# Kernel optimization log

Measured on AMD Instinct MI355X. Metric: run time of the kernel, lower is better.

Reference implementation:

```python
import jax, jax.numpy as jnp
import numpy as np

C = 320        # in_channels == inner_dim (n_heads*d_head = 8*40)
HEADS = 8
DH = 40
CTX = 768
FF_INNER = 1280  # 4*C
G = 32         # GroupNorm groups


def _ln(x, w, b, eps=1e-5):
    m = x.mean(-1, keepdims=True)
    v = ((x - m) ** 2).mean(-1, keepdims=True)
    return (x - m) * jax.lax.rsqrt(v + eps) * w + b


def _attn(q, k, v, heads, scale):
    # faithful to source: split last dim as (d h) -> head index is fastest
    B, Lq, D = q.shape
    Lk = k.shape[1]
    dh = D // heads
    q = q.reshape(B, Lq, dh, heads).transpose(0, 3, 1, 2)  # b h i d
    k = k.reshape(B, Lk, dh, heads).transpose(0, 3, 1, 2)  # b h j d
    v = v.reshape(B, Lk, dh, heads).transpose(0, 3, 1, 2)
    sim = jnp.einsum('bhid,bhjd->bhij', q, k) * scale
    w = jax.nn.softmax(sim, axis=-1)
    o = jnp.einsum('bhij,bhjd->bhid', w, v)
    # merge as (h d): head index is slowest on output (matches source)
    return o.transpose(0, 2, 1, 3).reshape(B, Lq, heads * dh)


def setup_inputs() -> dict:
    key = jax.random.key(0)
    ks = jax.random.split(key, 20)
    n = lambda i, shape: jax.random.normal(ks[i], shape, jnp.float32) * 0.02
    z = lambda d: jnp.zeros((d,), jnp.float32)
    o = lambda d: jnp.ones((d,), jnp.float32)
    return dict(
        x=jax.random.normal(ks[0], (1, C, 64, 64), jnp.float32),
        context=jax.random.normal(ks[1], (1, 77, CTX), jnp.float32),
        gn_w=o(C), gn_b=z(C),
        w_in=n(2, (C, C)), b_in=z(C),
        ln1_w=o(C), ln1_b=z(C),
        wq1=n(3, (C, C)), wk1=n(4, (C, C)), wv1=n(5, (C, C)),
        wo1=n(6, (C, C)), bo1=z(C),
        ln2_w=o(C), ln2_b=z(C),
        wq2=n(7, (C, C)), wk2=n(8, (CTX, C)), wv2=n(9, (CTX, C)),
        wo2=n(10, (C, C)), bo2=z(C),
        ln3_w=o(C), ln3_b=z(C),
        wff1=n(11, (C, 2 * FF_INNER)), bff1=z(2 * FF_INNER),
        wff2=n(12, (FF_INNER, C)), bff2=z(C),
        w_out=n(13, (C, C)), b_out=z(C),
    )


def reference(x, context, gn_w, gn_b, w_in, b_in,
              ln1_w, ln1_b, wq1, wk1, wv1, wo1, bo1,
              ln2_w, ln2_b, wq2, wk2, wv2, wo2, bo2,
              ln3_w, ln3_b, wff1, bff1, wff2, bff2,
              w_out, b_out):
    B, Cc, H, W = x.shape
    scale = DH ** (-0.5)
    x_in = x
    # GroupNorm(32, eps=1e-6)
    g = x.reshape(B, G, Cc // G, H, W)
    m = g.mean((2, 3, 4), keepdims=True)
    v = ((g - m) ** 2).mean((2, 3, 4), keepdims=True)
    h = ((g - m) * jax.lax.rsqrt(v + 1e-6)).reshape(B, Cc, H, W)
    h = h * gn_w[None, :, None, None] + gn_b[None, :, None, None]
    # 1x1 conv in_proj
    h = jnp.einsum('bchw,co->bohw', h, w_in) + b_in[None, :, None, None]
    # b c h w -> b (h w) c
    t = h.transpose(0, 2, 3, 1).reshape(B, H * W, C)
    # --- transformer block (depth=1) ---
    # attn_1: self-attn; NOTE source applies k/v proj to the QUERY projection
    hn = _ln(t, ln1_w, ln1_b)
    q = hn @ wq1
    k = q @ wk1
    vv = q @ wv1
    t = t + (_attn(q, k, vv, HEADS, scale) @ wo1 + bo1)
    # attn_2: cross-attn with context
    hn = _ln(t, ln2_w, ln2_b)
    q = hn @ wq2
    k = context @ wk2
    vv = context @ wv2
    t = t + (_attn(q, k, vv, HEADS, scale) @ wo2 + bo2)
    # GEGLU feed-forward
    hn = _ln(t, ln3_w, ln3_b)
    p = hn @ wff1 + bff1
    a, gate = p[..., :FF_INNER], p[..., FF_INNER:]
    t = t + ((a * jax.nn.gelu(gate, approximate=False)) @ wff2 + bff2)
    # b (h w) c -> b c h w
    s = t.reshape(B, H, W, C).transpose(0, 3, 1, 2)
    out = jnp.einsum('bchw,co->bohw', s, w_out) + b_out[None, :, None, None]
    return out + x_in
```

## Files before the change

### kernel.cpp

```cpp
#include <hip/hip_runtime.h>
#include <hip/hip_bf16.h>
#include <math.h>

#define CCH 320
#define NHEADS 8
#define DH 40
#define HW 4096
#define FFI 1280

typedef __bf16 bf16x8 __attribute__((ext_vector_type(8)));
typedef unsigned short u16x8 __attribute__((ext_vector_type(8)));
typedef short s16x4 __attribute__((ext_vector_type(4)));
typedef float f32x4 __attribute__((ext_vector_type(4)));
typedef unsigned int u32x4 __attribute__((ext_vector_type(4)));

__device__ inline unsigned short f2bf(float f) {
    __hip_bfloat16 h = __float2bfloat16(f);
    return __builtin_bit_cast(unsigned short, h);
}
__device__ inline unsigned pk2bf(float a, float b) {
#if __has_builtin(__builtin_amdgcn_cvt_pk_bf16_f32)
    typedef __bf16 bf16x2 __attribute__((ext_vector_type(2)));
    bf16x2 r = __builtin_amdgcn_cvt_pk_bf16_f32(a, b);
    return __builtin_bit_cast(unsigned, r);
#else
    return (unsigned)f2bf(a) | ((unsigned)f2bf(b) << 16);
#endif
}
__device__ inline float bf2f(unsigned short u) {
    return __builtin_bit_cast(float, ((unsigned)u) << 16);
}
__device__ inline bf16x8 ldfrag(const unsigned short* p) {
    u16x8 raw = *reinterpret_cast<const u16x8*>(p);
    return __builtin_bit_cast(bf16x8, raw);
}
__device__ inline s16x4 pk2frag(unsigned a, unsigned b) {
    unsigned long long v = (unsigned long long)a | ((unsigned long long)b << 32);
    return __builtin_bit_cast(s16x4, v);
}

__device__ inline float ex2(float x) {
#if __has_builtin(__builtin_amdgcn_exp2f)
    return __builtin_amdgcn_exp2f(x);
#else
    return exp2f(x);
#endif
}
__device__ inline float fast_rcp(float x) {
#if __has_builtin(__builtin_amdgcn_rcpf)
    return __builtin_amdgcn_rcpf(x);
#else
    return 1.f / x;
#endif
}
__device__ inline float fast_gelu(float x) {
    float z = fabsf(x) * 0.70710678118654752f;
    float t = fast_rcp(fmaf(0.3275911f, z, 1.f));
    float poly = fmaf(fmaf(fmaf(fmaf(1.061405429f, t, -1.453152027f), t,
                               1.421413741f), t, -0.284496736f), t,
                      0.254829592f) * t;
    float e = ex2(z * z * -1.4426950408889634f);
    float erfz = 1.f - poly * e;
    float s = copysignf(erfz, x);
    return 0.5f * x * (1.f + s);
}

__global__ __launch_bounds__(256) void prep_w2(
    const float* __restrict__ w_in, const float* __restrict__ wq1,
    const float* __restrict__ wk1, const float* __restrict__ wv1,
    const float* __restrict__ wo1, const float* __restrict__ wq2,
    const float* __restrict__ wo2, const float* __restrict__ w_out,
    const float* __restrict__ wff1, const float* __restrict__ wff2,
    const float* __restrict__ wk2, const float* __restrict__ wv2,
    unsigned short* __restrict__ Wt) {
    __shared__ float tile[64][65];
    const int b = blockIdx.x, tid = threadIdx.x;
    const float* src;
    int K, stride, dstoff, k0, n0;
    bool glu = false;
    if (b < 200) {
        int m = b / 25, t = b % 25;
        k0 = (t / 5) * 64; n0 = (t % 5) * 64;
        K = 320; stride = 320; dstoff = m * 102400;
        src = (m == 0) ? w_in : (m == 1) ? wq1 : (m == 2) ? wk1 :
              (m == 3) ? wv1 : (m == 4) ? wo1 : (m == 5) ? wq2 :
              (m == 6) ? wo2 : w_out;
    } else if (b < 300) {
        int t = b - 200;
        k0 = (t / 5) * 64; n0 = (t % 5) * 64;
        K = 1280; stride = 320; dstoff = 1638400; src = wff2;
    } else if (b < 500) {
        int t = b - 300;
        k0 = (t / 40) * 64; n0 = (t % 40) * 64;
        K = 320; stride = 2560; dstoff = 819200; src = wff1; glu = true;
    } else if (b < 560) {
        int t = b - 500;
        k0 = (t / 5) * 64; n0 = (t % 5) * 64;
        K = 768; stride = 320; dstoff = 2048000; src = wk2;
    } else {
        int t = b - 560;
        k0 = (t / 5) * 64; n0 = (t % 5) * 64;
        K = 768; stride = 320; dstoff = 2048000 + 245760; src = wv2;
    }
#pragma unroll
    for (int i = 0; i < 16; ++i) {
        int idx = tid + i * 256;
        int r = idx >> 6, cn = idx & 63;
        int scol = glu ? ((n0 >> 1) + (cn >> 1) + (cn & 1) * FFI) : (n0 + cn);
        tile[r][cn] = src[(size_t)(k0 + r) * stride + scol];
    }
    __syncthreads();
#pragma unroll
    for (int i = 0; i < 16; ++i) {
        int idx = tid + i * 256;
        int cl = idx >> 6, cr = idx & 63;
        Wt[dstoff + (size_t)(n0 + cl) * K + k0 + cr] = f2bf(tile[cr][cl]);
    }
}

__global__ void pack_ctx(const float* __restrict__ ctx,
                         unsigned short* __restrict__ D) {
    int idx = blockIdx.x * 256 + threadIdx.x;
    int row = idx / 768, col = idx - row * 768;
    float v = (row < 77) ? ctx[row * 768 + col] : 0.f;
    D[idx] = f2bf(v);
}

__global__ __launch_bounds__(256) void gn_stats(const float* __restrict__ X,
                                                float2* __restrict__ part) {
    __shared__ float s1[256], s2[256];
    const int b = blockIdx.x, tid = threadIdx.x;
    const float* xg = X + b * 5120;
    float s = 0.f, sq = 0.f;
#pragma unroll
    for (int i = 0; i < 20; ++i) { float v = xg[tid + i * 256]; s += v; sq += v * v; }
    s1[tid] = s; s2[tid] = sq; __syncthreads();
    for (int off = 128; off > 0; off >>= 1) {
        if (tid < off) { s1[tid] += s1[tid + off]; s2[tid] += s2[tid + off]; }
        __syncthreads();
    }
    if (tid == 0) part[b] = make_float2(s1[0], s2[0]);
}

__global__ __launch_bounds__(256) void gn_apply(const float* __restrict__ X,
                                                const float2* __restrict__ part,
                                                const float* __restrict__ w,
                                                const float* __restrict__ b,
                                                unsigned short* __restrict__ Y) {
    __shared__ float tile[64][65];
    __shared__ float gm[32], gr[32];
    const int tid = threadIdx.x;
    const int hw0 = blockIdx.x * 64, c0 = blockIdx.y * 64;
    if (tid < 32) {
        float s = 0.f, sq = 0.f;
#pragma unroll
        for (int i = 0; i < 8; ++i) { float2 p = part[tid * 8 + i]; s += p.x; sq += p.y; }
        float mean = s * (1.f / 40960.f);
        float var  = sq * (1.f / 40960.f) - mean * mean;
        gm[tid] = mean; gr[tid] = rsqrtf(var + 1e-6f);
    }
#pragma unroll
    for (int i = 0; i < 16; ++i) {
        int idx = tid + i * 256;
        int r = idx >> 6, col = idx & 63;
        tile[r][col] = X[(size_t)(c0 + r) * HW + hw0 + col];
    }
    __syncthreads();
#pragma unroll
    for (int i = 0; i < 16; ++i) {
        int idx = tid + i * 256;
        int hwl = idx >> 6, cl = idx & 63;
        int c = c0 + cl, g = c / 10;
        float v = (tile[cl][hwl] - gm[g]) * gr[g] * w[c] + b[c];
        Y[(size_t)(hw0 + hwl) * CCH + c] = f2bf(v);
    }
}

__global__ __launch_bounds__(256) void ln_kernel(const float* __restrict__ X,
                                                 const float* __restrict__ w,
                                                 const float* __restrict__ b,
                                                 unsigned short* __restrict__ Y) {
    const int row  = blockIdx.x * 4 + (threadIdx.x >> 6);
    const int lane = threadIdx.x & 63;
    const float* xr = X + row * CCH;
    float v[5];
    float s = 0.f, sq = 0.f;
#pragma unroll
    for (int i = 0; i < 5; ++i) { v[i] = xr[lane + 64 * i]; s += v[i]; sq += v[i] * v[i]; }
#pragma unroll
    for (int off = 32; off > 0; off >>= 1) {
        s  += __shfl_xor(s, off, 64);
        sq += __shfl_xor(sq, off, 64);
    }
    const float mean = s * (1.f / 320.f);
    const float var  = sq * (1.f / 320.f) - mean * mean;
    const float rstd = rsqrtf(var + 1e-5f);
    unsigned short* yr = Y + row * CCH;
#pragma unroll
    for (int i = 0; i < 5; ++i) {
        int c = lane + 64 * i;
        yr[c] = f2bf((v[i] - mean) * rstd * w[c] + b[c]);
    }
}

template <int MT, int K>
__global__ __launch_bounds__(256) void gemm4(
    const unsigned short* __restrict__ A,
    const unsigned short* __restrict__ Bt,
    const float* __restrict__ bias,
    const float* __restrict__ res,
    void* __restrict__ Cout, void* __restrict__ Cout2,
    int N, int mode, float scale) {
    constexpr int NCH = K / 64;
    __shared__ __align__(16) unsigned short Ab[2][MT * 16 * 64];
    __shared__ __align__(16) unsigned short Bb[2][64 * 64];
    const int tid  = threadIdx.x;
    const int wave = tid >> 6, lane = tid & 63;
    const int quad = lane >> 4, c = lane & 15;
    const int m0 = blockIdx.y * (MT * 16);
    const int bn = blockIdx.x;

    f32x4 acc[MT];
#pragma unroll
    for (int i = 0; i < MT; ++i) acc[i] = (f32x4){0.f, 0.f, 0.f, 0.f};

    const unsigned short* aslab = A + (size_t)m0 * K;
    const unsigned short* bslab = Bt + (size_t)(bn * 64) * K;

    constexpr int ITA = MT * 16 * 8 / 256;
    int arow[ITA], aoff[ITA];
#pragma unroll
    for (int i = 0; i < ITA; ++i) {
        int idx = tid + i * 256;
        arow[i] = idx >> 3;
        int g = idx & 7;
        aoff[i] = arow[i] * 64 + ((g ^ (arow[i] & 7)) * 8);
    }
    int brow[2], boff[2];
#pragma unroll
    for (int i = 0; i < 2; ++i) {
        int idx = tid + i * 256;
        brow[i] = idx >> 3;
        int g = idx & 7;
        boff[i] = brow[i] * 64 + ((g ^ (brow[i] & 7)) * 8);
    }
    const int ag = (tid & 7) * 8;

    {
        u16x8 ra[ITA], rb[2];
#pragma unroll
        for (int i = 0; i < ITA; ++i)
            ra[i] = *(const u16x8*)(aslab + (size_t)arow[i] * K + ag);
#pragma unroll
        for (int i = 0; i < 2; ++i)
            rb[i] = *(const u16x8*)(bslab + (size_t)brow[i] * K + ag);
#pragma unroll
        for (int i = 0; i < ITA; ++i) *(u16x8*)&Ab[0][aoff[i]] = ra[i];
#pragma unroll
        for (int i = 0; i < 2; ++i) *(u16x8*)&Bb[0][boff[i]] = rb[i];
    }
    __syncthreads();

    const int swz0 = (quad ^ (c & 7)) * 8;
    const int swz1 = ((quad + 4) ^ (c & 7)) * 8;
#pragma unroll
    for (int ch = 0; ch < NCH; ++ch) {
        const int buf = ch & 1;
        u16x8 ra[ITA], rb[2];
        if (ch + 1 < NCH) {
            const int kb = (ch + 1) * 64;
#pragma unroll
            for (int i = 0; i < ITA; ++i)
                ra[i] = *(const u16x8*)(aslab + (size_t)arow[i] * K + kb + ag);
#pragma unroll
            for (int i = 0; i < 2; ++i)
                rb[i] = *(const u16x8*)(bslab + (size_t)brow[i] * K + kb + ag);
        }
        bf16x8 b0 = ldfrag(&Bb[buf][(wave * 16 + c) * 64 + swz0]);
        bf16x8 b1 = ldfrag(&Bb[buf][(wave * 16 + c) * 64 + swz1]);
#pragma unroll
        for (int mt = 0; mt < MT; ++mt) {
            bf16x8 a0 = ldfrag(&Ab[buf][(mt * 16 + c) * 64 + swz0]);
            bf16x8 a1 = ldfrag(&Ab[buf][(mt * 16 + c) * 64 + swz1]);
            acc[mt] = __builtin_amdgcn_mfma_f32_16x16x32_bf16(a0, b0, acc[mt], 0, 0, 0);
            acc[mt] = __builtin_amdgcn_mfma_f32_16x16x32_bf16(a1, b1, acc[mt], 0, 0, 0);
        }
        if (ch + 1 < NCH) {
            const int nb = buf ^ 1;
#pragma unroll
            for (int i = 0; i < ITA; ++i) *(u16x8*)&Ab[nb][aoff[i]] = ra[i];
#pragma unroll
            for (int i = 0; i < 2; ++i) *(u16x8*)&Bb[nb][boff[i]] = rb[i];
        }
        __syncthreads();
    }

    const int col = bn * 64 + wave * 16 + c;
    float bval = 0.f;
    if (bias) bval = (mode == 5) ? bias[(col >> 1) + (col & 1) * FFI] : bias[col];

    if (mode == 9) {
#pragma unroll
        for (int mt = 0; mt < MT; ++mt) {
            const int row0 = m0 + mt * 16 + quad * 4;
            float4 xv = *(const float4*)(res + (size_t)col * HW + row0);
            float4 ov;
            ov.x = acc[mt][0] + bval + xv.x;
            ov.y = acc[mt][1] + bval + xv.y;
            ov.z = acc[mt][2] + bval + xv.z;
            ov.w = acc[mt][3] + bval + xv.w;
            *(float4*)((float*)Cout + (size_t)col * HW + row0) = ov;
        }
        return;
    }
#pragma unroll
    for (int mt = 0; mt < MT; ++mt) {
#pragma unroll
        for (int r = 0; r < 4; ++r) {
            const int row = m0 + mt * 16 + quad * 4 + r;
            float v = acc[mt][r];
            if (mode == 0) {
                v += bval;
                if (res) v += res[(size_t)row * N + col];
                ((float*)Cout)[(size_t)row * N + col] = v;
            } else if (mode == 2) {
                int h = col & 7, d = col >> 3;
                ((unsigned short*)Cout)[(((size_t)h << 12) + row) * 64 + d] = f2bf(v * scale);
            } else if (mode == 4) {
                ((unsigned short*)Cout)[(size_t)row * N + col] =
                    f2bf(v + bval + res[(size_t)row * N + col]);
            } else if (mode == 5) {
                v += bval;
                float other = __shfl_xor(v, 1, 64);
                if ((c & 1) == 0) {
                    float g = fast_gelu(other);
                    ((unsigned short*)Cout)[(size_t)row * FFI + (col >> 1)] = f2bf(v * g);
                }
            } else if (mode == 6) {
                ((unsigned short*)Cout)[(size_t)row * N + col] = f2bf(v);
                int h = col & 7, d = col >> 3;
                ((unsigned short*)Cout2)[(((size_t)h << 12) + row) * 64 + d] = f2bf(v * scale);
            } else if (mode == 7) {
                if (col < 320) {
                    int h = col & 7, d = col >> 3;
                    ((unsigned short*)Cout)[(((size_t)h << 12) + row) * 64 + d] = f2bf(v);
                } else {
                    int c2 = col - 320;
                    int h = c2 & 7, d = c2 >> 3;
                    ((unsigned short*)Cout2)[(((size_t)(h * 48 + d)) << 12) + row] = f2bf(v);
                }
            } else {
                if (col < 320) {
                    int h = col & 7, d = col >> 3;
                    ((unsigned short*)Cout)[(((size_t)h << 7) + row) * 64 + d] = f2bf(v);
                } else {
                    int c2 = col - 320;
                    int h = c2 & 7, d = c2 >> 3;
                    ((unsigned short*)Cout2)[(size_t)(h * 48 + d) * 128 + row] = f2bf(v);
                }
            }
        }
    }
}

__global__ void set_ones(unsigned short* __restrict__ Vt,
                         unsigned short* __restrict__ Vc) {
    int idx = blockIdx.x * 256 + threadIdx.x;
    if (idx < 32768) {
        int h = idx >> 12, r = idx & 4095;
        Vt[((size_t)(h * 48 + 40) << 12) + r] = 0x3F80;
    } else {
        int j = idx - 32768;
        int h = j >> 7, r = j & 127;
        Vc[(h * 48 + 40) * 128 + r] = 0x3F80;
    }
}

template <int TILES, bool MASK>
__global__ __launch_bounds__(256) void attn8(
    const unsigned short* __restrict__ Qp,
    const unsigned short* __restrict__ Kp,
    const unsigned short* __restrict__ Vt,
    float* __restrict__ pO, float* __restrict__ pL,
    int Lk, int Lkp) {
    __shared__ __align__(16) unsigned short Kb[2][64 * 64];
    __shared__ __align__(16) unsigned short Vb[2][48 * 64];
    const int tid  = threadIdx.x;
    const int wave = tid >> 6, lane = tid & 63;
    const int quad = lane >> 4, c = lane & 15;
    const int id  = blockIdx.x;
    const int h   = id & 7;
    const int qt  = (id >> 3) & 31;
    const int seg = id >> 8;
    const int q0  = qt * 128 + wave * 32;

    const unsigned short* qbaseA = Qp + ((((size_t)h << 12) + q0 + c) << 6) + quad * 8;
    const bf16x8 bQA0 = ldfrag(qbaseA);
    const bf16x8 bQA1 = ldfrag(qbaseA + 32);
    const bf16x8 bQB0 = ldfrag(qbaseA + 1024);
    const bf16x8 bQB1 = ldfrag(qbaseA + 1024 + 32);

    f32x4 oA[3], oB[3];
#pragma unroll
    for (int i = 0; i < 3; ++i) {
        oA[i] = (f32x4){0.f, 0.f, 0.f, 0.f};
        oB[i] = (f32x4){0.f, 0.f, 0.f, 0.f};
    }

    const int kt0 = seg * TILES;
    const unsigned short* kglob = Kp + (((size_t)h * Lkp + kt0 * 64) << 6);
    const unsigned short* vglob = Vt + ((size_t)h * 48) * Lkp + kt0 * 64;

    const int r0 = lane >> 3;
    const int g  = lane & 7;
    int ldsoff[4];
    const unsigned short* gptr0[4];
#pragma unroll
    for (int i = 0; i < 4; ++i) {
        int s = wave + 4 * i;
        if (s < 8) {
            int row = s * 8 + r0;
            ldsoff[i] = row * 64 + (g ^ (row & 7)) * 8;
            gptr0[i]  = kglob + (size_t)row * 64 + g * 8;
        } else if (s < 14) {
            int d = (s - 8) * 8 + r0;
            ldsoff[i] = d * 64 + (g ^ (d & 7)) * 8;
            gptr0[i]  = vglob + (size_t)d * Lkp + g * 8;
        } else {
            ldsoff[i] = 0; gptr0[i] = nullptr;
        }
    }
    const bool isK[4] = {(wave + 0) < 8, (wave + 4) < 8, (wave + 8) < 8, (wave + 12) < 8};
    const bool act[4] = {true, true, true, (wave + 12) < 14};

    {
        u16x8 st[4];
#pragma unroll
        for (int i = 0; i < 4; ++i)
            if (act[i]) st[i] = *(const u16x8*)(gptr0[i]);
#pragma unroll
        for (int i = 0; i < 4; ++i)
            if (act[i]) {
                unsigned short* lp = isK[i] ? &Kb[0][ldsoff[i]] : &Vb[0][ldsoff[i]];
                *(u16x8*)lp = st[i];
            }
    }
    __syncthreads();

#pragma unroll
    for (int t = 0; t < TILES; ++t) {
        const int b = t & 1;
        u16x8 st[4];
        if (t + 1 < TILES) {
            const int kb = (t + 1) * 64;
#pragma unroll
            for (int i = 0; i < 4; ++i)
                if (act[i]) {
                    const unsigned short* gp =
                        isK[i] ? (gptr0[i] + (size_t)kb * 64) : (gptr0[i] + kb);
                    st[i] = *(const u16x8*)gp;
                }
        }
        const unsigned short* Kl = &Kb[b][0];
        const unsigned short* Vl = &Vb[b][0];
        const int sw0 = (quad ^ (c & 7)) * 8;
        const int sw1 = ((quad + 4) ^ (c & 7)) * 8;
        f32x4 sA[4], sB[4];
        __builtin_amdgcn_s_setprio(1);
#pragma unroll
        for (int blk = 0; blk < 4; ++blk) {
            const int row = (blk * 16 + c) * 64;
            bf16x8 k0 = ldfrag(Kl + row + sw0);
            bf16x8 k1 = ldfrag(Kl + row + sw1);
            f32x4 zA = {0.f, 0.f, 0.f, 0.f};
            zA = __builtin_amdgcn_mfma_f32_16x16x32_bf16(k0, bQA0, zA, 0, 0, 0);
            zA = __builtin_amdgcn_mfma_f32_16x16x32_bf16(k1, bQA1, zA, 0, 0, 0);
            sA[blk] = zA;
            f32x4 zB = {0.f, 0.f, 0.f, 0.f};
            zB = __builtin_amdgcn_mfma_f32_16x16x32_bf16(k0, bQB0, zB, 0, 0, 0);
            zB = __builtin_amdgcn_mfma_f32_16x16x32_bf16(k1, bQB1, zB, 0, 0, 0);
            sB[blk] = zB;
        }
        __builtin_amdgcn_s_setprio(0);
        if (MASK) {
            const int abs_kb = kt0 * 64 + t * 64;
#pragma unroll
            for (int blk = 0; blk < 4; ++blk)
#pragma unroll
                for (int r = 0; r < 4; ++r) {
                    bool inv = (abs_kb + blk * 16 + quad * 4 + r >= Lk);
                    sA[blk][r] = inv ? -30000.f : sA[blk][r];
                    sB[blk][r] = inv ? -30000.f : sB[blk][r];
                }
        }
        s16x4 PA[4], PB[4];
#pragma unroll
        for (int blk = 0; blk < 4; ++blk) {
            PA[blk] = pk2frag(pk2bf(ex2(sA[blk][0]), ex2(sA[blk][1])),
                              pk2bf(ex2(sA[blk][2]), ex2(sA[blk][3])));
            PB[blk] = pk2frag(pk2bf(ex2(sB[blk][0]), ex2(sB[blk][1])),
                              pk2bf(ex2(sB[blk][2]), ex2(sB[blk][3])));
        }
        __builtin_amdgcn_s_setprio(1);
#pragma unroll
        for (int db = 0; db < 3; ++db) {
            const int dim = db * 16 + c;
            const unsigned short* vrow = Vl + dim * 64;
            const int dswz = dim & 7;
#pragma unroll
            for (int kb = 0; kb < 4; ++kb) {
                const int off = (((kb * 2 + (quad >> 1)) ^ dswz) * 8) + (quad & 1) * 4;
                s16x4 vf = *(const s16x4*)(vrow + off);
                oA[db] = __builtin_amdgcn_mfma_f32_16x16x16bf16_1k(vf, PA[kb], oA[db], 0, 0, 0);
                oB[db] = __builtin_amdgcn_mfma_f32_16x16x16bf16_1k(vf, PB[kb], oB[db], 0, 0, 0);
            }
        }
        __builtin_amdgcn_s_setprio(0);
        if (t + 1 < TILES) {
            const int nb = b ^ 1;
#pragma unroll
            for (int i = 0; i < 4; ++i)
                if (act[i]) {
                    unsigned short* lp = isK[i] ? &Kb[nb][ldsoff[i]] : &Vb[nb][ldsoff[i]];
                    *(u16x8*)lp = st[i];
                }
        }
        __syncthreads();
    }
    const size_t base = ((size_t)(seg * 8 + h)) << 12;
    float* obA = pO + (base + q0 + c) * 40;
    *(float4*)(obA + quad * 4)      = make_float4(oA[0][0], oA[0][1], oA[0][2], oA[0][3]);
    *(float4*)(obA + 16 + quad * 4) = make_float4(oA[1][0], oA[1][1], oA[1][2], oA[1][3]);
    if (quad < 2)
        *(float4*)(obA + 32 + quad * 4) = make_float4(oA[2][0], oA[2][1], oA[2][2], oA[2][3]);
    float* obB = pO + (base + q0 + 16 + c) * 40;
    *(float4*)(obB + quad * 4)      = make_float4(oB[0][0], oB[0][1], oB[0][2], oB[0][3]);
    *(float4*)(obB + 16 + quad * 4) = make_float4(oB[1][0], oB[1][1], oB[1][2], oB[1][3]);
    if (quad < 2)
        *(float4*)(obB + 32 + quad * 4) = make_float4(oB[2][0], oB[2][1], oB[2][2], oB[2][3]);
    if (quad == 2) {
        pL[base + q0 + c]      = oA[2][0];
        pL[base + q0 + 16 + c] = oB[2][0];
    }
}

__global__ __launch_bounds__(256) void attn_combine2(
    const float* __restrict__ pO, const float* __restrict__ pL,
    unsigned short* __restrict__ O, int S) {
    int idx = blockIdx.x * 256 + threadIdx.x;
    int h = idx / (HW * 10);
    int rem = idx - h * (HW * 10);
    int row = rem / 10, dg = rem - row * 10;
    float4 num = make_float4(0.f, 0.f, 0.f, 0.f);
    float den = 0.f;
    for (int s = 0; s < S; ++s) {
        size_t base = ((size_t)(s * 8 + h)) << 12;
        float4 p = *(const float4*)(pO + (base + row) * 40 + dg * 4);
        num.x += p.x; num.y += p.y; num.z += p.z; num.w += p.w;
        den += pL[base + row];
    }
    float inv = fast_rcp(den);
    unsigned short* ob = O + (size_t)row * CCH + h * DH + dg * 4;
    unsigned lo = pk2bf(num.x * inv, num.y * inv);
    unsigned hi = pk2bf(num.z * inv, num.w * inv);
    *(uint2*)ob = make_uint2(lo, hi);
}

extern "C" void kernel_launch(void* const* d_in, const int* in_sizes, int n_in,
                              void* d_out, int out_size, void* d_ws, size_t ws_size,
                              hipStream_t stream) {
    const float* x     = (const float*)d_in[0];
    const float* ctx   = (const float*)d_in[1];
    const float* gn_w  = (const float*)d_in[2];
    const float* gn_b  = (const float*)d_in[3];
    const float* w_in  = (const float*)d_in[4];
    const float* b_in  = (const float*)d_in[5];
    const float* ln1_w = (const float*)d_in[6];
    const float* ln1_b = (const float*)d_in[7];
    const float* wq1   = (const float*)d_in[8];
    const float* wk1   = (const float*)d_in[9];
    const float* wv1   = (const float*)d_in[10];
    const float* wo1   = (const float*)d_in[11];
    const float* bo1   = (const float*)d_in[12];
    const float* ln2_w = (const float*)d_in[13];
    const float* ln2_b = (const float*)d_in[14];
    const float* wq2   = (const float*)d_in[15];
    const float* wk2   = (const float*)d_in[16];
    const float* wv2   = (const float*)d_in[17];
    const float* wo2   = (const float*)d_in[18];
    const float* bo2   = (const float*)d_in[19];
    const float* ln3_w = (const float*)d_in[20];
    const float* ln3_b = (const float*)d_in[21];
    const float* wff1  = (const float*)d_in[22];
    const float* bff1  = (const float*)d_in[23];
    const float* wff2  = (const float*)d_in[24];
    const float* bff2  = (const float*)d_in[25];
    const float* w_out = (const float*)d_in[26];
    const float* b_out = (const float*)d_in[27];
    float* out = (float*)d_out;

    const int NT = HW * CCH;
    float* ws = (float*)d_ws;
    float* t_   = ws;
    float* y_   = t_ + NT;
    float* pO   = y_ + NT;
    float* pL   = pO + 4 * 8 * 4096 * 40;
    float2* gnp = (float2*)(pL + 4 * 8 * 4096);
    unsigned short* u = (unsigned short*)(gnp + 256);
    unsigned short* a_bf = u;                  u += NT;
    unsigned short* q_bf = u;                  u += NT;
    unsigned short* o_bf = u;                  u += NT;
    unsigned short* t_bf = u;                  u += NT;
    unsigned short* g_bf = u;                  u += HW * FFI;
    unsigned short* Qp   = u;                  u += 8 * 4096 * 64;
    unsigned short* Kp   = u;                  u += 8 * 4096 * 64;
    unsigned short* Vt   = u;                  u += 8 * 48 * 4096;
    unsigned short* Kc   = u;                  u += 8 * 128 * 64;
    unsigned short* Vc   = u;                  u += 8 * 48 * 128;
    unsigned short* Wt   = u;                  u += 2048000 + 2 * 245760;
    unsigned short* ctx_bf = u;                u += 128 * 768;

    const unsigned short* w_inT  = Wt;
    const unsigned short* wq1T   = Wt + 102400;
    const unsigned short* wk1T   = Wt + 204800;
    const unsigned short* wo1T   = Wt + 409600;
    const unsigned short* wq2T   = Wt + 512000;
    const unsigned short* wo2T   = Wt + 614400;
    const unsigned short* w_outT = Wt + 716800;
    const unsigned short* wff1T  = Wt + 819200;
    const unsigned short* wff2T  = Wt + 1638400;
    const unsigned short* wk2T   = Wt + 2048000;

    const float qscale = 0.15811388300841897f * 1.4426950408889634f;

    prep_w2<<<620, 256, 0, stream>>>(w_in, wq1, wk1, wv1, wo1, wq2, wo2, w_out,
                                     wff1, wff2, wk2, wv2, Wt);
    hipMemsetAsync(Qp, 0,
                   (size_t)(8 * 4096 * 64 * 2 + 8 * 48 * 4096 + 8 * 128 * 64 + 8 * 48 * 128) * 2,
                   stream);
    set_ones<<<132, 256, 0, stream>>>(Vt, Vc);
    pack_ctx<<<384, 256, 0, stream>>>(ctx, ctx_bf);

    gn_stats<<<256, 256, 0, stream>>>(x, gnp);
    gn_apply<<<dim3(64, 5), 256, 0, stream>>>(x, gnp, gn_w, gn_b, a_bf);
    gemm4<2, 320><<<dim3(5, 128), 256, 0, stream>>>(a_bf, w_inT, b_in, nullptr, t_, nullptr, CCH, 0, 1.f);
    ln_kernel<<<1024, 256, 0, stream>>>(t_, ln1_w, ln1_b, a_bf);
    gemm4<2, 320><<<dim3(5, 128), 256, 0, stream>>>(a_bf, wq1T, nullptr, nullptr, q_bf, Qp, CCH, 6, qscale);
    gemm4<2, 320><<<dim3(10, 128), 256, 0, stream>>>(q_bf, wk1T, nullptr, nullptr, Kp, Vt, 640, 7, 1.f);
    attn8<16, false><<<1024, 256, 0, stream>>>(Qp, Kp, Vt, pO, pL, HW, HW);
    attn_combine2<<<1280, 256, 0, stream>>>(pO, pL, o_bf, 4);
    gemm4<2, 320><<<dim3(5, 128), 256, 0, stream>>>(o_bf, wo1T, bo1, t_, t_, nullptr, CCH, 0, 1.f);
    ln_kernel<<<1024, 256, 0, stream>>>(t_, ln2_w, ln2_b, a_bf);
    gemm4<2, 320><<<dim3(5, 128), 256, 0, stream>>>(a_bf, wq2T, nullptr, nullptr, Qp, nullptr, CCH, 2, qscale);
    gemm4<2, 768><<<dim3(10, 4), 256, 0, stream>>>(ctx_bf, wk2T, nullptr, nullptr, Kc, Vc, 640, 8, 1.f);
    attn8<2, true><<<256, 256, 0, stream>>>(Qp, Kc, Vc, pO, pL, 77, 128);
    attn_combine2<<<1280, 256, 0, stream>>>(pO, pL, o_bf, 1);
    gemm4<2, 320><<<dim3(5, 128), 256, 0, stream>>>(o_bf, wo2T, bo2, t_, t_, nullptr, CCH, 0, 1.f);
    ln_kernel<<<1024, 256, 0, stream>>>(t_, ln3_w, ln3_b, a_bf);
    gemm4<2, 320><<<dim3(40, 128), 256, 0, stream>>>(a_bf, wff1T, bff1, nullptr, g_bf, nullptr, 2 * FFI, 5, 1.f);
    gemm4<2, 1280><<<dim3(5, 128), 256, 0, stream>>>(g_bf, wff2T, bff2, t_, t_bf, nullptr, CCH, 4, 1.f);
    gemm4<2, 320><<<dim3(5, 128), 256, 0, stream>>>(t_bf, w_outT, b_out, x, out, nullptr, CCH, 9, 1.f);
}
```

Measured before the change: 300.3 us.

## Fuse attention pad init into GEMM epilogues, finalize cross-attn in kernel

Drops the large memset and set_ones launch by having the Q/K/V projection epilogues write the zero padding and ones column directly. Cross-attention, which runs as a single segment, now normalizes and writes bf16 output itself, removing an attn_combine launch. LayerNorm uses vectorized float4 loads and packed bf16 stores, and two GEMMs switch to taller M tiles. The epilogues now do extra scattered stores, and correctness depends on the padding being fully covered.

```diff
diff --git a/kernel.cpp b/kernel.cpp
--- a/kernel.cpp
+++ b/kernel.cpp
@@ -183,10 +183,12 @@
     const int row  = blockIdx.x * 4 + (threadIdx.x >> 6);
     const int lane = threadIdx.x & 63;
     const float* xr = X + row * CCH;
-    float v[5];
+    const float4 a = *(const float4*)(xr + lane * 4);
+    const float  e = xr[256 + lane];
+    float v[5] = {a.x, a.y, a.z, a.w, e};
     float s = 0.f, sq = 0.f;
 #pragma unroll
-    for (int i = 0; i < 5; ++i) { v[i] = xr[lane + 64 * i]; s += v[i]; sq += v[i] * v[i]; }
+    for (int i = 0; i < 5; ++i) { s += v[i]; sq += v[i] * v[i]; }
 #pragma unroll
     for (int off = 32; off > 0; off >>= 1) {
         s  += __shfl_xor(s, off, 64);
@@ -196,11 +198,15 @@
     const float var  = sq * (1.f / 320.f) - mean * mean;
     const float rstd = rsqrtf(var + 1e-5f);
     unsigned short* yr = Y + row * CCH;
-#pragma unroll
-    for (int i = 0; i < 5; ++i) {
-        int c = lane + 64 * i;
-        yr[c] = f2bf((v[i] - mean) * rstd * w[c] + b[c]);
-    }
+    const float4 w4 = *(const float4*)(w + lane * 4);
+    const float4 b4 = *(const float4*)(b + lane * 4);
+    float r0 = (v[0] - mean) * rstd * w4.x + b4.x;
+    float r1 = (v[1] - mean) * rstd * w4.y + b4.y;
+    float r2 = (v[2] - mean) * rstd * w4.z + b4.z;
+    float r3 = (v[3] - mean) * rstd * w4.w + b4.w;
+    *(uint2*)(yr + lane * 4) = make_uint2(pk2bf(r0, r1), pk2bf(r2, r3));
+    int ct = 256 + lane;
+    yr[ct] = f2bf((v[4] - mean) * rstd * w[ct] + b[ct]);
 }
 
 template <int MT, int K>
@@ -326,6 +332,8 @@
             } else if (mode == 2) {
                 int h = col & 7, d = col >> 3;
                 ((unsigned short*)Cout)[(((size_t)h << 12) + row) * 64 + d] = f2bf(v * scale);
+                if (d < 24)
+                    ((unsigned short*)Cout)[(((size_t)h << 12) + row) * 64 + 40 + d] = 0;
             } else if (mode == 4) {
                 ((unsigned short*)Cout)[(size_t)row * N + col] =
                     f2bf(v + bval + res[(size_t)row * N + col]);
@@ -340,48 +348,48 @@
                 ((unsigned short*)Cout)[(size_t)row * N + col] = f2bf(v);
                 int h = col & 7, d = col >> 3;
                 ((unsigned short*)Cout2)[(((size_t)h << 12) + row) * 64 + d] = f2bf(v * scale);
+                if (d < 24)
+                    ((unsigned short*)Cout2)[(((size_t)h << 12) + row) * 64 + 40 + d] = 0;
             } else if (mode == 7) {
                 if (col < 320) {
                     int h = col & 7, d = col >> 3;
                     ((unsigned short*)Cout)[(((size_t)h << 12) + row) * 64 + d] = f2bf(v);
+                    if (d < 24)
+                        ((unsigned short*)Cout)[(((size_t)h << 12) + row) * 64 + 40 + d] = 0;
                 } else {
                     int c2 = col - 320;
                     int h = c2 & 7, d = c2 >> 3;
                     ((unsigned short*)Cout2)[(((size_t)(h * 48 + d)) << 12) + row] = f2bf(v);
+                    if (d < 8)
+                        ((unsigned short*)Cout2)[(((size_t)(h * 48 + 40 + d)) << 12) + row] =
+                            (d == 0) ? (unsigned short)0x3F80 : (unsigned short)0;
                 }
             } else {
                 if (col < 320) {
                     int h = col & 7, d = col >> 3;
                     ((unsigned short*)Cout)[(((size_t)h << 7) + row) * 64 + d] = f2bf(v);
+                    if (d < 24)
+                        ((unsigned short*)Cout)[(((size_t)h << 7) + row) * 64 + 40 + d] = 0;
                 } else {
                     int c2 = col - 320;
                     int h = c2 & 7, d = c2 >> 3;
                     ((unsigned short*)Cout2)[(size_t)(h * 48 + d) * 128 + row] = f2bf(v);
+                    if (d < 8)
+                        ((unsigned short*)Cout2)[(size_t)(h * 48 + 40 + d) * 128 + row] =
+                            (d == 0) ? (unsigned short)0x3F80 : (unsigned short)0;
                 }
             }
         }
     }
 }
 
-__global__ void set_ones(unsigned short* __restrict__ Vt,
-                         unsigned short* __restrict__ Vc) {
-    int idx = blockIdx.x * 256 + threadIdx.x;
-    if (idx < 32768) {
-        int h = idx >> 12, r = idx & 4095;
-        Vt[((size_t)(h * 48 + 40) << 12) + r] = 0x3F80;
-    } else {
-        int j = idx - 32768;
-        int h = j >> 7, r = j & 127;
-        Vc[(h * 48 + 40) * 128 + r] = 0x3F80;
-    }
-}
-
-template <int TILES, bool MASK>
+template <int TILES, bool MASK, bool FINAL>
 __global__ __launch_bounds__(256) void attn8(
     const unsigned short* __restrict__ Qp,
     const unsigned short* __restrict__ Kp,
     const unsigned short* __restrict__ Vt,
     float* __restrict__ pO, float* __restrict__ pL,
+    unsigned short* __restrict__ Ofin,
     int Lk, int Lkp) {
     __shared__ __align__(16) unsigned short Kb[2][64 * 64];
     __shared__ __align__(16) unsigned short Vb[2][48 * 64];
@@ -526,6 +534,34 @@
                 }
         }
         __syncthreads();
+    }
+    if (FINAL) {
+        float lA = __shfl(oA[2][0], 32 + c, 64);
+        float lB = __shfl(oB[2][0], 32 + c, 64);
+        float liA = fast_rcp(lA), liB = fast_rcp(lB);
+        unsigned short* oaptr = Ofin + (size_t)(q0 + c) * CCH + h * DH;
+        unsigned short* obptr = Ofin + (size_t)(q0 + 16 + c) * CCH + h * DH;
+        *(uint2*)(oaptr + quad * 4) =
+            make_uint2(pk2bf(oA[0][0] * liA, oA[0][1] * liA),
+                       pk2bf(oA[0][2] * liA, oA[0][3] * liA));
+        *(uint2*)(oaptr + 16 + quad * 4) =
+            make_uint2(pk2bf(oA[1][0] * liA, oA[1][1] * liA),
+                       pk2bf(oA[1][2] * liA, oA[1][3] * liA));
+        if (quad < 2)
+            *(uint2*)(oaptr + 32 + quad * 4) =
+                make_uint2(pk2bf(oA[2][0] * liA, oA[2][1] * liA),
+                           pk2bf(oA[2][2] * liA, oA[2][3] * liA));
+        *(uint2*)(obptr + quad * 4) =
+            make_uint2(pk2bf(oB[0][0] * liB, oB[0][1] * liB),
+                       pk2bf(oB[0][2] * liB, oB[0][3] * liB));
+        *(uint2*)(obptr + 16 + quad * 4) =
+            make_uint2(pk2bf(oB[1][0] * liB, oB[1][1] * liB),
+                       pk2bf(oB[1][2] * liB, oB[1][3] * liB));
+        if (quad < 2)
+            *(uint2*)(obptr + 32 + quad * 4) =
+                make_uint2(pk2bf(oB[2][0] * liB, oB[2][1] * liB),
+                           pk2bf(oB[2][2] * liB, oB[2][3] * liB));
+        return;
     }
     const size_t base = ((size_t)(seg * 8 + h)) << 12;
     float* obA = pO + (base + q0 + c) * 40;
@@ -635,10 +671,6 @@
 
     prep_w2<<<620, 256, 0, stream>>>(w_in, wq1, wk1, wv1, wo1, wq2, wo2, w_out,
                                      wff1, wff2, wk2, wv2, Wt);
-    hipMemsetAsync(Qp, 0,
-                   (size_t)(8 * 4096 * 64 * 2 + 8 * 48 * 4096 + 8 * 128 * 64 + 8 * 48 * 128) * 2,
-                   stream);
-    set_ones<<<132, 256, 0, stream>>>(Vt, Vc);
     pack_ctx<<<384, 256, 0, stream>>>(ctx, ctx_bf);
 
     gn_stats<<<256, 256, 0, stream>>>(x, gnp);
@@ -646,18 +678,17 @@
     gemm4<2, 320><<<dim3(5, 128), 256, 0, stream>>>(a_bf, w_inT, b_in, nullptr, t_, nullptr, CCH, 0, 1.f);
     ln_kernel<<<1024, 256, 0, stream>>>(t_, ln1_w, ln1_b, a_bf);
     gemm4<2, 320><<<dim3(5, 128), 256, 0, stream>>>(a_bf, wq1T, nullptr, nullptr, q_bf, Qp, CCH, 6, qscale);
-    gemm4<2, 320><<<dim3(10, 128), 256, 0, stream>>>(q_bf, wk1T, nullptr, nullptr, Kp, Vt, 640, 7, 1.f);
-    attn8<16, false><<<1024, 256, 0, stream>>>(Qp, Kp, Vt, pO, pL, HW, HW);
+    gemm4<4, 320><<<dim3(10, 64), 256, 0, stream>>>(q_bf, wk1T, nullptr, nullptr, Kp, Vt, 640, 7, 1.f);
+    attn8<16, false, false><<<1024, 256, 0, stream>>>(Qp, Kp, Vt, pO, pL, nullptr, HW, HW);
     attn_combine2<<<1280, 256, 0, stream>>>(pO, pL, o_bf, 4);
     gemm4<2, 320><<<dim3(5, 128), 256, 0, stream>>>(o_bf, wo1T, bo1, t_, t_, nullptr, CCH, 0, 1.f);
     ln_kernel<<<1024, 256, 0, stream>>>(t_, ln2_w, ln2_b, a_bf);
     gemm4<2, 320><<<dim3(5, 128), 256, 0, stream>>>(a_bf, wq2T, nullptr, nullptr, Qp, nullptr, CCH, 2, qscale);
     gemm4<2, 768><<<dim3(10, 4), 256, 0, stream>>>(ctx_bf, wk2T, nullptr, nullptr, Kc, Vc, 640, 8, 1.f);
-    attn8<2, true><<<256, 256, 0, stream>>>(Qp, Kc, Vc, pO, pL, 77, 128);
-    attn_combine2<<<1280, 256, 0, stream>>>(pO, pL, o_bf, 1);
+    attn8<2, true, true><<<256, 256, 0, stream>>>(Qp, Kc, Vc, nullptr, nullptr, o_bf, 77, 128);
     gemm4<2, 320><<<dim3(5, 128), 256, 0, stream>>>(o_bf, wo2T, bo2, t_, t_, nullptr, CCH, 0, 1.f);
     ln_kernel<<<1024, 256, 0, stream>>>(t_, ln3_w, ln3_b, a_bf);
-    gemm4<2, 320><<<dim3(40, 128), 256, 0, stream>>>(a_bf, wff1T, bff1, nullptr, g_bf, nullptr, 2 * FFI, 5, 1.f);
+    gemm4<4, 320><<<dim3(40, 64), 256, 0, stream>>>(a_bf, wff1T, bff1, nullptr, g_bf, nullptr, 2 * FFI, 5, 1.f);
     gemm4<2, 1280><<<dim3(5, 128), 256, 0, stream>>>(g_bf, wff2T, bff2, t_, t_bf, nullptr, CCH, 4, 1.f);
     gemm4<2, 320><<<dim3(5, 128), 256, 0, stream>>>(t_bf, w_outT, b_out, x, out, nullptr, CCH, 9, 1.f);
 }
```

Result: no change. 304.1 us (+1.3%).
